# Optimization experiments

Hardware: AMD Instinct MI355X
Metric: run time of the kernel (lower is better)

The kernel has to match this reference:

```python
import jax, jax.numpy as jnp
import numpy as np

DIM = 1024
NUM_HEADS = 16
HEAD_DIM = DIM // NUM_HEADS
SCALE = HEAD_DIM ** -0.5


def setup_inputs() -> dict:
    key = jax.random.key(0)
    k_x, k_qkv, k_pw, k_pb = jax.random.split(key, 4)
    B, S = 2, 2048
    x = jax.random.normal(k_x, (B, S, DIM), dtype=jnp.float32)
    # nn.Linear(dim, 3*dim, bias=False): weight [3*dim, dim]
    w_qkv = jax.random.normal(k_qkv, (3 * DIM, DIM), dtype=jnp.float32) * (DIM ** -0.5)
    # nn.Linear(dim, dim): weight [dim, dim], bias [dim]
    w_proj = jax.random.normal(k_pw, (DIM, DIM), dtype=jnp.float32) * (DIM ** -0.5)
    b_proj = jax.random.normal(k_pb, (DIM,), dtype=jnp.float32) * 0.01
    return {"x": x, "w_qkv": w_qkv, "w_proj": w_proj, "b_proj": b_proj}


def reference(x, w_qkv, w_proj, b_proj):
    B, S, D = x.shape
    qkv = jnp.einsum("bsd,ed->bse", x, w_qkv)  # [B,S,3D]
    q, k, v = jnp.split(qkv, 3, axis=-1)
    def heads(t):  # [B,S,D] -> [B,H,S,hd]
        return t.reshape(B, S, NUM_HEADS, HEAD_DIM).transpose(0, 2, 1, 3)
    q, k, v = heads(q), heads(k), heads(v)
    attn = jnp.einsum("bhqd,bhkd->bhqk", q, k) * SCALE  # [B,H,S,S]
    attn = jax.nn.softmax(attn, axis=-1)
    out = jnp.einsum("bhqk,bhkd->bhqd", attn, v)  # [B,H,S,hd]
    out = out.transpose(0, 2, 1, 3).reshape(B, S, D)
    return jnp.einsum("bsd,ed->bse", out, w_proj) + b_proj
```

## Files before the change

### kernel.cpp

```cpp
#include <hip/hip_runtime.h>
#include <stdint.h>

typedef __bf16 bf16;
typedef __bf16 bf16x8 __attribute__((ext_vector_type(8)));
typedef float f32x4 __attribute__((ext_vector_type(4)));
typedef float f32x16 __attribute__((ext_vector_type(16)));

typedef __attribute__((address_space(1))) void gvoid_t;
typedef __attribute__((address_space(3))) void lvoid_t;

__device__ __forceinline__ void gload16(const void* src, void* lds) {
    __builtin_amdgcn_global_load_lds((gvoid_t*)src, (lvoid_t*)lds, 16, 0, 0);
}

__device__ __forceinline__ float fexp2(float x) {
    float r;
    asm("v_exp_f32 %0, %1" : "=v"(r) : "v"(x));
    return r;
}

__global__ __launch_bounds__(256) void cvt3_kernel(const float* __restrict__ x,
                                                   const float* __restrict__ wqkv,
                                                   const float* __restrict__ wproj,
                                                   bf16* __restrict__ xb,
                                                   bf16* __restrict__ wqkvb,
                                                   bf16* __restrict__ wprojb) {
    int idx = blockIdx.x * 256 + threadIdx.x;
    int stride = gridDim.x * 256;
    for (int i = idx; i < 1048576; i += stride) {
        const float* in;
        bf16* out;
        int j;
        if (i < 524288) { in = x; out = xb; j = i; }
        else if (i < 917504) { in = wqkv; out = wqkvb; j = i - 524288; }
        else { in = wproj; out = wprojb; j = i - 917504; }
        const float4* p = (const float4*)in;
        float4 a = p[(long)j * 2], b = p[(long)j * 2 + 1];
        bf16x8 o;
        o[0] = (bf16)a.x; o[1] = (bf16)a.y; o[2] = (bf16)a.z; o[3] = (bf16)a.w;
        o[4] = (bf16)b.x; o[5] = (bf16)b.y; o[6] = (bf16)b.z; o[7] = (bf16)b.w;
        ((bf16x8*)out)[j] = o;
    }
}

template <bool F32OUT, int BN>
__global__ __launch_bounds__(256) void gemm_bt(const bf16* __restrict__ A,
                                               const bf16* __restrict__ W,
                                               const float* __restrict__ bias,
                                               void* __restrict__ Cout,
                                               const int M, const int N, const int K) {
    constexpr int NT = BN / 32;
    constexpr int BELEMS = BN * 32;
    __shared__ __align__(16) bf16 Alds[3 * 4096];
    __shared__ __align__(16) bf16 Blds[3 * BELEMS];
    const int t = threadIdx.x;
    const int wid = t >> 6, lane = t & 63;
    const int g = lane >> 4, c = lane & 15;
    const int wm = wid >> 1, wn = wid & 1;
    const long bm = (long)blockIdx.y * 128, bn = (long)blockIdx.x * BN;

    f32x4 acc[4][NT] = {};

    const int arow = t >> 2;
    const int acol = (t & 3) * 8;
    const bf16* Asrc = A + (bm + arow) * (long)K + acol;
    const bf16* Bsrc = W + (bn + arow) * (long)K + acol;
    const int dstb = wid * 512;

#define GSTAGE(BI)                                                       \
    {                                                                    \
        bf16* ad = Alds + (BI) * 4096 + dstb;                            \
        bf16* bd = Blds + (BI) * BELEMS + dstb;                          \
        gload16(Asrc, ad);                                               \
        gload16(Asrc + (long)64 * K, ad + 2048);                         \
        gload16(Bsrc, bd);                                               \
        if constexpr (BN == 128) gload16(Bsrc + (long)64 * K, bd + 2048);\
        Asrc += 32;                                                      \
        Bsrc += 32;                                                      \
    }

    auto computeg = [&](int bi) __attribute__((always_inline)) {
        const bf16* Ab = Alds + bi * 4096;
        const bf16* Bb = Blds + bi * BELEMS;
        bf16x8 af[4], bfr[NT];
#pragma unroll
        for (int mt = 0; mt < 4; ++mt)
            af[mt] = *(const bf16x8*)(Ab + (wm * 64 + mt * 16 + c) * 32 + g * 8);
#pragma unroll
        for (int nt = 0; nt < NT; ++nt)
            bfr[nt] = *(const bf16x8*)(Bb + (wn * (BN / 2) + nt * 16 + c) * 32 + g * 8);
#pragma unroll
        for (int mt = 0; mt < 4; ++mt)
#pragma unroll
            for (int nt = 0; nt < NT; ++nt)
                acc[mt][nt] = __builtin_amdgcn_mfma_f32_16x16x32_bf16(af[mt], bfr[nt],
                                                                      acc[mt][nt], 0, 0, 0);
    };

#define GWAITN                                                              \
    if constexpr (BN == 128) { asm volatile("s_waitcnt vmcnt(4)" ::: "memory"); } \
    else { asm volatile("s_waitcnt vmcnt(3)" ::: "memory"); }

#define GSTEP(CUR, NXT)            \
    GWAITN;                        \
    __builtin_amdgcn_s_barrier();  \
    GSTAGE(NXT);                   \
    computeg(CUR);

    GSTAGE(0);
    GSTAGE(1);
    for (int t3 = 0; t3 < 10; ++t3) {
        GSTEP(0, 2)
        GSTEP(1, 0)
        GSTEP(2, 1)
    }
    GWAITN;
    __builtin_amdgcn_s_barrier();
    computeg(0);
    asm volatile("s_waitcnt vmcnt(0)" ::: "memory");
    __builtin_amdgcn_s_barrier();
    computeg(1);
#undef GSTEP
#undef GWAITN
#undef GSTAGE

#pragma unroll
    for (int mt = 0; mt < 4; ++mt) {
#pragma unroll
        for (int nt = 0; nt < NT; ++nt) {
#pragma unroll
            for (int i = 0; i < 4; ++i) {
                const long row = bm + wm * 64 + mt * 16 + g * 4 + i;
                const long col = bn + wn * (BN / 2) + nt * 16 + c;
                if constexpr (F32OUT) {
                    ((float*)Cout)[row * N + col] = acc[mt][nt][i] + bias[col];
                } else {
                    ((bf16*)Cout)[row * N + col] = (bf16)acc[mt][nt][i];
                }
            }
        }
    }
}

__global__ __launch_bounds__(128) void flash_kernel(const bf16* __restrict__ qk,
                                                    const bf16* __restrict__ Vt,
                                                    bf16* __restrict__ P0,
                                                    bf16* __restrict__ P1,
                                                    float* __restrict__ lpar) {
    __shared__ __align__(16) bf16 KV[24576];

    const int t = threadIdx.x;
    const int wid = t >> 6, lane = t & 63;
    const int l31 = lane & 31, hl = lane >> 5;

    const int i0 = blockIdx.x;
    const int xcd = i0 & 7, slot = i0 >> 3;
    const int bh = xcd * 4 + (slot >> 5);
    const int rem = slot & 31;
    const int qb = rem >> 1, kvh = rem & 1;
    const int b = bh >> 4, h = bh & 15;
    const int rowbase = b * 2048;
    const int q0w = qb * 128 + wid * 64;

    bf16x8 qfa[4], qfb[4];
    {
        const bf16* qra = qk + (long)(rowbase + q0w + l31) * 2048 + h * 64 + hl * 8;
        const bf16* qrb = qra + 32 * 2048;
        const float qs = 0.18033688f;
#pragma unroll
        for (int ks = 0; ks < 4; ++ks) {
            bf16x8 a = *(const bf16x8*)(qra + ks * 16);
            bf16x8 d = *(const bf16x8*)(qrb + ks * 16);
#pragma unroll
            for (int e = 0; e < 8; ++e) {
                qfa[ks][e] = (bf16)((float)a[e] * qs);
                qfb[ks][e] = (bf16)((float)d[e] * qs);
            }
        }
    }

    const int srow0 = wid * 8 + ((lane >> 3) & 7);
    const int swcol = ((lane & 7) ^ (srow0 & 7)) * 8;
    const bf16* ksn = qk + (long)(rowbase + kvh * 1024 + srow0) * 2048 + 1024 + h * 64 + swcol;
    const bf16* vsn = Vt + (long)(h * 64 + srow0) * 4096 + b * 2048 + kvh * 1024 + swcol;
    const int kchunk = wid * 512;

    int rdoff[4];
#pragma unroll
    for (int ks = 0; ks < 4; ++ks)
        rdoff[ks] = l31 * 64 + (((ks * 2 + hl) ^ (l31 & 7)) * 8);

    float lpA0 = 0.f, lpB0 = 0.f, lpA1 = 0.f, lpB1 = 0.f;
    f32x16 oacc00 = {}, oacc10 = {}, oacc01 = {}, oacc11 = {};

#define STAGE(BI)                                                        \
    {                                                                    \
        bf16* kd = KV + (BI) * 4096 + kchunk;                            \
        bf16* vd = KV + 12288 + (BI) * 4096 + kchunk;                    \
        gload16(ksn, kd);                                                \
        gload16(ksn + 32768, kd + 1024);                                 \
        gload16(ksn + 65536, kd + 2048);                                 \
        gload16(ksn + 98304, kd + 3072);                                 \
        gload16(vsn, vd);                                                \
        gload16(vsn + 65536, vd + 1024);                                 \
        gload16(vsn + 131072, vd + 2048);                                \
        gload16(vsn + 196608, vd + 3072);                                \
        ksn += 131072;                                                   \
        vsn += 64;                                                       \
    }

    auto compute = [&](int bi) __attribute__((always_inline)) {
        const bf16* Kb = KV + bi * 4096;
        const bf16* Vb = KV + 12288 + bi * 4096;
        f32x16 s00 = {}, s10 = {}, s01 = {}, s11 = {};
        __builtin_amdgcn_s_setprio(1);
#pragma unroll
        for (int ks = 0; ks < 4; ++ks) {
            bf16x8 kf0 = *(const bf16x8*)(Kb + rdoff[ks]);
            bf16x8 kf1 = *(const bf16x8*)(Kb + 2048 + rdoff[ks]);
            s00 = __builtin_amdgcn_mfma_f32_32x32x16_bf16(kf0, qfa[ks], s00, 0, 0, 0);
            s10 = __builtin_amdgcn_mfma_f32_32x32x16_bf16(kf1, qfa[ks], s10, 0, 0, 0);
            s01 = __builtin_amdgcn_mfma_f32_32x32x16_bf16(kf0, qfb[ks], s01, 0, 0, 0);
            s11 = __builtin_amdgcn_mfma_f32_32x32x16_bf16(kf1, qfb[ks], s11, 0, 0, 0);
        }
        __builtin_amdgcn_s_setprio(0);
        float p00[16], p10[16], p01[16], p11[16];
#pragma unroll
        for (int r = 0; r < 16; ++r) p00[r] = fexp2(s00[r]);
#pragma unroll
        for (int r = 0; r < 16; ++r) p10[r] = fexp2(s10[r]);
#pragma unroll
        for (int r = 0; r < 16; ++r) p01[r] = fexp2(s01[r]);
#pragma unroll
        for (int r = 0; r < 16; ++r) p11[r] = fexp2(s11[r]);
#pragma unroll
        for (int r = 0; r < 8; ++r) {
            lpA0 += p00[r] + p10[r];
            lpB0 += p00[r + 8] + p10[r + 8];
            lpA1 += p01[r] + p11[r];
            lpB1 += p01[r + 8] + p11[r + 8];
        }
        __builtin_amdgcn_s_setprio(1);
#pragma unroll
        for (int ks = 0; ks < 4; ++ks) {
            bf16x8 vf0 = *(const bf16x8*)(Vb + rdoff[ks]);
            bf16x8 vf1 = *(const bf16x8*)(Vb + 2048 + rdoff[ks]);
            const int s = (ks & 1) * 8;
            {
                const float* pp = (ks < 2) ? p00 : p10;
                unsigned wA, wB, wC, wD;
                asm("v_cvt_pk_bf16_f32 %0, %1, %2" : "=v"(wA) : "v"(pp[s + 0]), "v"(pp[s + 1]));
                asm("v_cvt_pk_bf16_f32 %0, %1, %2" : "=v"(wB) : "v"(pp[s + 4]), "v"(pp[s + 5]));
                asm("v_cvt_pk_bf16_f32 %0, %1, %2" : "=v"(wC) : "v"(pp[s + 2]), "v"(pp[s + 3]));
                asm("v_cvt_pk_bf16_f32 %0, %1, %2" : "=v"(wD) : "v"(pp[s + 6]), "v"(pp[s + 7]));
                asm("v_permlane32_swap_b32 %0, %1" : "+v"(wA), "+v"(wB));
                asm("v_permlane32_swap_b32 %0, %1" : "+v"(wC), "+v"(wD));
                union { unsigned w[4]; bf16x8 v; } pu;
                pu.w[0] = wA; pu.w[1] = wC; pu.w[2] = wB; pu.w[3] = wD;
                oacc00 = __builtin_amdgcn_mfma_f32_32x32x16_bf16(pu.v, vf0, oacc00, 0, 0, 0);
                oacc10 = __builtin_amdgcn_mfma_f32_32x32x16_bf16(pu.v, vf1, oacc10, 0, 0, 0);
            }
            {
                const float* pp = (ks < 2) ? p01 : p11;
                unsigned wA, wB, wC, wD;
                asm("v_cvt_pk_bf16_f32 %0, %1, %2" : "=v"(wA) : "v"(pp[s + 0]), "v"(pp[s + 1]));
                asm("v_cvt_pk_bf16_f32 %0, %1, %2" : "=v"(wB) : "v"(pp[s + 4]), "v"(pp[s + 5]));
                asm("v_cvt_pk_bf16_f32 %0, %1, %2" : "=v"(wC) : "v"(pp[s + 2]), "v"(pp[s + 3]));
                asm("v_cvt_pk_bf16_f32 %0, %1, %2" : "=v"(wD) : "v"(pp[s + 6]), "v"(pp[s + 7]));
                asm("v_permlane32_swap_b32 %0, %1" : "+v"(wA), "+v"(wB));
                asm("v_permlane32_swap_b32 %0, %1" : "+v"(wC), "+v"(wD));
                union { unsigned w[4]; bf16x8 v; } pu;
                pu.w[0] = wA; pu.w[1] = wC; pu.w[2] = wB; pu.w[3] = wD;
                oacc01 = __builtin_amdgcn_mfma_f32_32x32x16_bf16(pu.v, vf0, oacc01, 0, 0, 0);
                oacc11 = __builtin_amdgcn_mfma_f32_32x32x16_bf16(pu.v, vf1, oacc11, 0, 0, 0);
            }
        }
        __builtin_amdgcn_s_setprio(0);
    };

    STAGE(0);
    STAGE(1);

#define FSTEP(CUR, NXT)                                    \
    asm volatile("s_waitcnt vmcnt(8)" ::: "memory");       \
    __builtin_amdgcn_s_barrier();                          \
    STAGE(NXT);                                            \
    compute(CUR);

    for (int t3 = 0; t3 < 4; ++t3) {
        FSTEP(0, 2)
        FSTEP(1, 0)
        FSTEP(2, 1)
    }
    FSTEP(0, 2)
    FSTEP(1, 0)
    asm volatile("s_waitcnt vmcnt(8)" ::: "memory");
    __builtin_amdgcn_s_barrier();
    compute(2);
    asm volatile("s_waitcnt vmcnt(0)" ::: "memory");
    __builtin_amdgcn_s_barrier();
    compute(0);
#undef FSTEP
#undef STAGE

    float lp0 = lpA0 + lpB0;
    float lp1 = lpA1 + lpB1;
    lp0 += __shfl_xor(lp0, 32);
    lp1 += __shfl_xor(lp1, 32);
    if (lane < 32) {
        const int qloc = qb * 128 + wid * 64 + l31;
        float* lp = lpar + kvh * 65536 + bh * 2048 + qloc;
        lp[0] = lp0;
        lp[32] = lp1;
    }

    bf16* Pd = kvh ? P1 : P0;
#pragma unroll
    for (int r = 0; r < 16; ++r) {
        const int qrow = (r & 3) + 8 * (r >> 2) + 4 * hl;
        const long rb0 = (long)(rowbase + q0w + qrow) * 1024 + h * 64 + l31;
        const long rb1 = (long)(rowbase + q0w + 32 + qrow) * 1024 + h * 64 + l31;
        Pd[rb0] = (bf16)oacc00[r];
        Pd[rb0 + 32] = (bf16)oacc10[r];
        Pd[rb1] = (bf16)oacc01[r];
        Pd[rb1 + 32] = (bf16)oacc11[r];
    }
}

__global__ __launch_bounds__(256) void combine_kernel(bf16* __restrict__ P0,
                                                      const bf16* __restrict__ P1,
                                                      const float* __restrict__ lpar) {
    int idx = blockIdx.x * 256 + threadIdx.x;
    int stride = gridDim.x * 256;
    for (int gi = idx; gi < 524288; gi += stride) {
        const int e0 = gi * 8;
        const int row = e0 >> 10, col = e0 & 1023;
        const int li = ((row >> 11) * 16 + (col >> 6)) * 2048 + (row & 2047);
        const float inv = 1.0f / (lpar[li] + lpar[li + 65536]);
        bf16x8 a = ((const bf16x8*)P0)[gi];
        bf16x8 b8 = ((const bf16x8*)P1)[gi];
        bf16x8 o;
#pragma unroll
        for (int e = 0; e < 8; ++e)
            o[e] = (bf16)(((float)a[e] + (float)b8[e]) * inv);
        ((bf16x8*)P0)[gi] = o;
    }
}

extern "C" void kernel_launch(void* const* d_in, const int* in_sizes, int n_in,
                              void* d_out, int out_size, void* d_ws, size_t ws_size,
                              hipStream_t stream) {
    const float* x = (const float*)d_in[0];
    const float* wqkv = (const float*)d_in[1];
    const float* wproj = (const float*)d_in[2];
    const float* bproj = (const float*)d_in[3];

    char* ws = (char*)d_ws;
    bf16* xb     = (bf16*)(ws);
    bf16* P1     = (bf16*)(ws);
    bf16* wqkvb  = (bf16*)(ws + 8388608);
    float* lpar  = (float*)(ws + 8388608);
    bf16* wprojb = (bf16*)(ws + 14680064);
    bf16* qk     = (bf16*)(ws + 16777216);
    bf16* Vt     = (bf16*)(ws + 33554432);
    bf16* attno  = (bf16*)(ws + 41943040);
    if (ws_size < 50331648) return;

    cvt3_kernel<<<2048, 256, 0, stream>>>(x, wqkv, wproj, xb, wqkvb, wprojb);

    gemm_bt<false, 128><<<dim3(16, 32), 256, 0, stream>>>(xb, wqkvb, nullptr, qk,
                                                          4096, 2048, 1024);

    gemm_bt<false, 64><<<dim3(64, 8), 256, 0, stream>>>(wqkvb + 2048 * 1024, xb, nullptr, Vt,
                                                        1024, 4096, 1024);

    flash_kernel<<<1024, 128, 0, stream>>>(qk, Vt, attno, P1, lpar);

    combine_kernel<<<1024, 256, 0, stream>>>(attno, P1, lpar);

    gemm_bt<true, 64><<<dim3(16, 32), 256, 0, stream>>>(attno, wprojb, bproj, d_out,
                                                        4096, 1024, 1024);
}
```

Baseline: 131.5 us.

## Grow flash attention blocks to four waves sharing each K/V tile

Result: no change. 133.2 us (+1.3%).

```diff
diff --git a/kernel.cpp b/kernel.cpp
--- a/kernel.cpp
+++ b/kernel.cpp
@@ -98,8 +98,11 @@
     };
 
 #define GWAITN                                                              \
-    if constexpr (BN == 128) { asm volatile("s_waitcnt vmcnt(4)" ::: "memory"); } \
-    else { asm volatile("s_waitcnt vmcnt(3)" ::: "memory"); }
+    if constexpr (BN == 128) {                                              \
+        asm volatile("s_waitcnt vmcnt(4) lgkmcnt(0)" ::: "memory");         \
+    } else {                                                                \
+        asm volatile("s_waitcnt vmcnt(3) lgkmcnt(0)" ::: "memory");         \
+    }
 
 #define GSTEP(CUR, NXT)            \
     GWAITN;                        \
@@ -117,7 +120,7 @@
     GWAITN;
     __builtin_amdgcn_s_barrier();
     computeg(0);
-    asm volatile("s_waitcnt vmcnt(0)" ::: "memory");
+    asm volatile("s_waitcnt vmcnt(0) lgkmcnt(0)" ::: "memory");
     __builtin_amdgcn_s_barrier();
     computeg(1);
 #undef GSTEP
@@ -142,7 +145,7 @@
     }
 }
 
-__global__ __launch_bounds__(128) void flash_kernel(const bf16* __restrict__ qk,
+__global__ __launch_bounds__(256) void flash_kernel(const bf16* __restrict__ qk,
                                                     const bf16* __restrict__ Vt,
                                                     bf16* __restrict__ P0,
                                                     bf16* __restrict__ P1,
@@ -155,12 +158,12 @@
 
     const int i0 = blockIdx.x;
     const int xcd = i0 & 7, slot = i0 >> 3;
-    const int bh = xcd * 4 + (slot >> 5);
-    const int rem = slot & 31;
+    const int bh = xcd * 4 + (slot >> 4);
+    const int rem = slot & 15;
     const int qb = rem >> 1, kvh = rem & 1;
     const int b = bh >> 4, h = bh & 15;
     const int rowbase = b * 2048;
-    const int q0w = qb * 128 + wid * 64;
+    const int q0w = qb * 256 + wid * 64;
 
     bf16x8 qfa[4], qfb[4];
     {
@@ -179,10 +182,10 @@
         }
     }
 
-    const int srow0 = wid * 8 + ((lane >> 3) & 7);
-    const int swcol = ((lane & 7) ^ (srow0 & 7)) * 8;
-    const bf16* ksn = qk + (long)(rowbase + kvh * 1024 + srow0) * 2048 + 1024 + h * 64 + swcol;
-    const bf16* vsn = Vt + (long)(h * 64 + srow0) * 4096 + b * 2048 + kvh * 1024 + swcol;
+    const int srow = t >> 3, sq = t & 7;
+    const int swcol = (sq ^ (srow & 7)) * 8;
+    const bf16* ksn = qk + (long)(rowbase + kvh * 1024 + srow) * 2048 + 1024 + h * 64 + swcol;
+    const bf16* vsn = Vt + (long)(h * 64 + srow) * 4096 + b * 2048 + kvh * 1024 + swcol;
     const int kchunk = wid * 512;
 
     int rdoff[4];
@@ -198,13 +201,9 @@
         bf16* kd = KV + (BI) * 4096 + kchunk;                            \
         bf16* vd = KV + 12288 + (BI) * 4096 + kchunk;                    \
         gload16(ksn, kd);                                                \
-        gload16(ksn + 32768, kd + 1024);                                 \
         gload16(ksn + 65536, kd + 2048);                                 \
-        gload16(ksn + 98304, kd + 3072);                                 \
         gload16(vsn, vd);                                                \
-        gload16(vsn + 65536, vd + 1024);                                 \
         gload16(vsn + 131072, vd + 2048);                                \
-        gload16(vsn + 196608, vd + 3072);                                \
         ksn += 131072;                                                   \
         vsn += 64;                                                       \
     }
@@ -281,10 +280,10 @@
     STAGE(0);
     STAGE(1);
 
-#define FSTEP(CUR, NXT)                                    \
-    asm volatile("s_waitcnt vmcnt(8)" ::: "memory");       \
-    __builtin_amdgcn_s_barrier();                          \
-    STAGE(NXT);                                            \
+#define FSTEP(CUR, NXT)                                                  \
+    asm volatile("s_waitcnt vmcnt(4) lgkmcnt(0)" ::: "memory");          \
+    __builtin_amdgcn_s_barrier();                                        \
+    STAGE(NXT);                                                          \
     compute(CUR);
 
     for (int t3 = 0; t3 < 4; ++t3) {
@@ -294,10 +293,10 @@
     }
     FSTEP(0, 2)
     FSTEP(1, 0)
-    asm volatile("s_waitcnt vmcnt(8)" ::: "memory");
+    asm volatile("s_waitcnt vmcnt(4) lgkmcnt(0)" ::: "memory");
     __builtin_amdgcn_s_barrier();
     compute(2);
-    asm volatile("s_waitcnt vmcnt(0)" ::: "memory");
+    asm volatile("s_waitcnt vmcnt(0) lgkmcnt(0)" ::: "memory");
     __builtin_amdgcn_s_barrier();
     compute(0);
 #undef FSTEP
@@ -308,8 +307,7 @@
     lp0 += __shfl_xor(lp0, 32);
     lp1 += __shfl_xor(lp1, 32);
     if (lane < 32) {
-        const int qloc = qb * 128 + wid * 64 + l31;
-        float* lp = lpar + kvh * 65536 + bh * 2048 + qloc;
+        float* lp = lpar + kvh * 65536 + bh * 2048 + q0w + l31;
         lp[0] = lp0;
         lp[32] = lp1;
     }
@@ -374,7 +372,7 @@
     gemm_bt<false, 64><<<dim3(64, 8), 256, 0, stream>>>(wqkvb + 2048 * 1024, xb, nullptr, Vt,
                                                         1024, 4096, 1024);
 
-    flash_kernel<<<1024, 128, 0, stream>>>(qk, Vt, attno, P1, lpar);
+    flash_kernel<<<512, 256, 0, stream>>>(qk, Vt, attno, P1, lpar);
 
     combine_kernel<<<1024, 256, 0, stream>>>(attno, P1, lpar);
 
```
